# Performance work log

Hardware: AMD Instinct MI355X
Metric: run time of the kernel (lower is better)

Reference implementation:

```python
import jax, jax.numpy as jnp
import numpy as np

EMBED_DIM = 1024
NUM_HEADS = 16
HEAD_DIM = EMBED_DIM // NUM_HEADS
ALPHA = 0.5  # mirror_bias['alpha'] default


def setup_inputs() -> dict:
    key = jax.random.key(0)
    k_x, k_m, kq, kk, kv, ko = jax.random.split(key, 6)
    B, S = 2, 2048
    x = jax.random.normal(k_x, (B, S, EMBED_DIM), dtype=jnp.float32)
    mask = jax.random.bernoulli(k_m, 0.1, (B, S))  # True = masked-out key (padding)
    # xavier_uniform for square [E,E]: limit = sqrt(6/(E+E))
    lim = float(np.sqrt(6.0 / (EMBED_DIM + EMBED_DIM)))
    Wq = jax.random.uniform(kq, (EMBED_DIM, EMBED_DIM), jnp.float32, -lim, lim)
    Wk = jax.random.uniform(kk, (EMBED_DIM, EMBED_DIM), jnp.float32, -lim, lim)
    Wv = jax.random.uniform(kv, (EMBED_DIM, EMBED_DIM), jnp.float32, -lim, lim)
    Wo = jax.random.uniform(ko, (EMBED_DIM, EMBED_DIM), jnp.float32, -lim, lim)
    return {"x": x, "Wq": Wq, "Wk": Wk, "Wv": Wv, "Wo": Wo, "mask": mask}


def _heads(t, B, S):
    # [B,S,E] -> [B,H,S,D]
    return t.reshape(B, S, NUM_HEADS, HEAD_DIM).transpose(0, 2, 1, 3)


def reference(x, Wq, Wk, Wv, Wo, mask):
    B, S, E = x.shape
    # nn.Linear(bias=False): y = x @ W.T
    q = _heads(x @ Wq.T, B, S)
    k = _heads(x @ Wk.T, B, S)
    v = _heads(x @ Wv.T, B, S)
    scores = jnp.einsum('bhqd,bhkd->bhqk', q, k) / jnp.sqrt(jnp.float32(HEAD_DIM))
    # mirror positional bias: target j = S-1-i
    i_idx = jnp.arange(S)[:, None]
    j_idx = jnp.arange(S)[None, :]
    dist = jnp.abs(j_idx - (S - 1 - i_idx)).astype(jnp.float32)
    bias = -ALPHA * (dist / jnp.float32(S))  # [S_q, S_k]
    scores = scores + bias[None, None, :, :]
    # bool 2D mask -> key padding mask [B,1,1,S_k], True = -inf
    scores = jnp.where(mask[:, None, None, :], -jnp.inf, scores)
    attn = jax.nn.softmax(scores, axis=-1)
    out = jnp.einsum('bhqk,bhkd->bhqd', attn, v)
    out = out.transpose(0, 2, 1, 3).reshape(B, S, E)
    return out @ Wo.T
```

## Files before the change

### kernel.cpp

```cpp
#include <hip/hip_runtime.h>

typedef unsigned short u16;
typedef unsigned int u32;
typedef unsigned long long u64;
typedef __attribute__((ext_vector_type(8))) short bf16x8;
typedef __attribute__((ext_vector_type(4))) float f32x4;
typedef __attribute__((ext_vector_type(2))) unsigned int u32x2;
typedef __attribute__((ext_vector_type(4))) unsigned int u32x4;

#define MFMA16(A, B, C) __builtin_amdgcn_mfma_f32_16x16x32_bf16(A, B, C, 0, 0, 0)

__device__ __forceinline__ u16 f2bf(float f) {
  union { float f; unsigned u; } x; x.f = f;
  unsigned r = x.u + 0x7fffu + ((x.u >> 16) & 1u);
  return (u16)(r >> 16);
}

__device__ __forceinline__ u32 pack_bf2(float a, float b) {
  u32 r;
  asm("v_cvt_pk_bf16_f32 %0, %1, %2" : "=v"(r) : "v"(a), "v"(b));
  return r;
}

__device__ __forceinline__ void gload_lds16(const u16* g, u16* l) {
  __builtin_amdgcn_global_load_lds((const __attribute__((address_space(1))) void*)g,
                                   (__attribute__((address_space(3))) void*)l,
                                   16, 0, 0);
}

__global__ __launch_bounds__(256) void cvt_all(const float* __restrict__ x,
                                               const float* __restrict__ Wq,
                                               const float* __restrict__ Wk,
                                               const float* __restrict__ Wv,
                                               const float* __restrict__ Wo,
                                               const int* __restrict__ mask,
                                               u16* __restrict__ xb,
                                               u16* __restrict__ Wqkvb,
                                               u16* __restrict__ Wob,
                                               float* __restrict__ Mbg,
                                               int NE, int NW, int NB) {
  if ((int)blockIdx.x == NB) {
    const int t = threadIdx.x;
    const int j0 = t * 16;
    const float K3C = -8.0f * 1.44269504f;
    const float KMS = K3C - 1.0e6f;
#pragma unroll
    for (int jj = 0; jj < 16; jj += 4) {
      const int4 m4 = *(const int4*)(mask + j0 + jj);
      float4 o;
      o.x = m4.x ? KMS : K3C;
      o.y = m4.y ? KMS : K3C;
      o.z = m4.z ? KMS : K3C;
      o.w = m4.w ? KMS : K3C;
      *(float4*)(Mbg + j0 + jj) = o;
    }
    return;
  }
  const int e = (blockIdx.x * 256 + threadIdx.x) * 8;
  const float* s;
  u16* d;
  if (e < NE) { s = x + e; d = xb + e; }
  else {
    int f = e - NE;
    if (f < 3 * NW) {
      d = Wqkvb + f;
      s = (f < NW) ? Wq + f : (f < 2 * NW) ? Wk + (f - NW) : Wv + (f - 2 * NW);
    } else { f -= 3 * NW; s = Wo + f; d = Wob + f; }
  }
  const float4 a = *(const float4*)s;
  const float4 b = *(const float4*)(s + 4);
  bf16x8 o;
  o[0] = (short)f2bf(a.x); o[1] = (short)f2bf(a.y);
  o[2] = (short)f2bf(a.z); o[3] = (short)f2bf(a.w);
  o[4] = (short)f2bf(b.x); o[5] = (short)f2bf(b.y);
  o[6] = (short)f2bf(b.z); o[7] = (short)f2bf(b.w);
  *(bf16x8*)d = o;
}

__global__ __launch_bounds__(256) void gemm_qkv(const u16* __restrict__ A,
                                                const u16* __restrict__ B,
                                                u16* __restrict__ Qo,
                                                u16* __restrict__ Ko,
                                                u16* __restrict__ Vto,
                                                int M, int N, int K) {
  __shared__ alignas(16) u16 As[128 * 64];
  __shared__ alignas(16) u16 Bs[128 * 64];
  const int t = threadIdx.x;
  const int lane = t & 63, wave = t >> 6;
  const int quad = lane >> 4, l16 = lane & 15;
  const int bid = blockIdx.x;
  const int swz = (bid & 7) * 96 + (bid >> 3);
  const int m0 = (swz / 24) * 128, n0 = (swz % 24) * 128;
  const int wm = (wave >> 1) * 64, wn = (wave & 1) * 64;
  const int sx = l16 & 7;

  f32x4 acc[4][4] = {};

  for (int kk = 0; kk < K; kk += 64) {
#pragma unroll
    for (int i = 0; i < 4; i++) {
      const int c = t + i * 256;
      const int row = c >> 3, sub = c & 7;
      const int col = ((sub ^ (row & 7)) * 8);
      gload_lds16(A + (size_t)(m0 + row) * K + kk + col, As + (size_t)c * 8);
      gload_lds16(B + (size_t)(n0 + row) * K + kk + col, Bs + (size_t)c * 8);
    }
    __syncthreads();

#pragma unroll
    for (int ks = 0; ks < 2; ks++) {
      bf16x8 af[4], bfr[4];
#pragma unroll
      for (int i = 0; i < 4; i++)
        af[i] = *(const bf16x8*)(As + (wm + i * 16 + l16) * 64 +
                                 ((ks * 4 + quad) ^ sx) * 8);
#pragma unroll
      for (int j = 0; j < 4; j++)
        bfr[j] = *(const bf16x8*)(Bs + (wn + j * 16 + l16) * 64 +
                                  ((ks * 4 + quad) ^ sx) * 8);
#pragma unroll
      for (int i = 0; i < 4; i++)
#pragma unroll
        for (int j = 0; j < 4; j++)
          acc[i][j] = MFMA16(af[i], bfr[j], acc[i][j]);
    }
    __syncthreads();
  }

  const int G = ((m0 + wm) & 2047) >> 6;
#pragma unroll
  for (int j = 0; j < 4; j++) {
    const int col = n0 + wn + j * 16 + l16;
    if (col < 1024) {
#pragma unroll
      for (int i = 0; i < 4; i++)
#pragma unroll
        for (int r = 0; r < 4; r++)
          Qo[(size_t)(m0 + wm + i * 16 + quad * 4 + r) * 1024 + col] =
              f2bf(acc[i][j][r]);
    } else if (col < 2048) {
#pragma unroll
      for (int i = 0; i < 4; i++)
#pragma unroll
        for (int r = 0; r < 4; r++)
          Ko[(size_t)(m0 + wm + i * 16 + quad * 4 + r) * 1024 + (col - 1024)] =
              f2bf(acc[i][j][r]);
    } else {
      u16* base = Vto + ((size_t)(m0 >> 11) * 1024 + (col - 2048)) * 2048 + G * 64;
      const int C = 8 * (quad & 1) + 16 * (quad >> 1);
      u32x4 w0, w1;
      w0.x = pack_bf2(acc[0][j][0], acc[0][j][1]);
      w0.y = pack_bf2(acc[0][j][2], acc[0][j][3]);
      w0.z = pack_bf2(acc[1][j][0], acc[1][j][1]);
      w0.w = pack_bf2(acc[1][j][2], acc[1][j][3]);
      w1.x = pack_bf2(acc[2][j][0], acc[2][j][1]);
      w1.y = pack_bf2(acc[2][j][2], acc[2][j][3]);
      w1.z = pack_bf2(acc[3][j][0], acc[3][j][1]);
      w1.w = pack_bf2(acc[3][j][2], acc[3][j][3]);
      *(u32x4*)(base + C) = w0;
      *(u32x4*)(base + C + 32) = w1;
    }
  }
}

__global__ __launch_bounds__(256) void gemm_out(const u16* __restrict__ A,
                                                const u16* __restrict__ B,
                                                float* __restrict__ C,
                                                int M, int N, int K) {
  __shared__ alignas(16) u16 As[128 * 64];
  __shared__ alignas(16) u16 Bs[64 * 64];
  const int t = threadIdx.x;
  const int lane = t & 63, wave = t >> 6;
  const int quad = lane >> 4, l16 = lane & 15;
  const int bid = blockIdx.x;
  const int swz = (bid & 7) * 64 + (bid >> 3);
  const int m0 = (swz >> 4) * 128, n0 = (swz & 15) * 64;
  const int wm = (wave >> 1) * 64, wn = (wave & 1) * 32;
  const int sx = l16 & 7;

  f32x4 acc[4][2] = {};

  for (int kk = 0; kk < K; kk += 64) {
#pragma unroll
    for (int i = 0; i < 4; i++) {
      const int c = t + i * 256;
      const int row = c >> 3, sub = c & 7;
      gload_lds16(A + (size_t)(m0 + row) * K + kk + ((sub ^ (row & 7)) * 8),
                  As + (size_t)c * 8);
    }
#pragma unroll
    for (int i = 0; i < 2; i++) {
      const int c = t + i * 256;
      const int row = c >> 3, sub = c & 7;
      gload_lds16(B + (size_t)(n0 + row) * K + kk + ((sub ^ (row & 7)) * 8),
                  Bs + (size_t)c * 8);
    }
    __syncthreads();

#pragma unroll
    for (int ks = 0; ks < 2; ks++) {
      bf16x8 af[4], bfr[2];
#pragma unroll
      for (int i = 0; i < 4; i++)
        af[i] = *(const bf16x8*)(As + (wm + i * 16 + l16) * 64 +
                                 ((ks * 4 + quad) ^ sx) * 8);
#pragma unroll
      for (int j = 0; j < 2; j++)
        bfr[j] = *(const bf16x8*)(Bs + (wn + j * 16 + l16) * 64 +
                                  ((ks * 4 + quad) ^ sx) * 8);
#pragma unroll
      for (int i = 0; i < 4; i++)
#pragma unroll
        for (int j = 0; j < 2; j++)
          acc[i][j] = MFMA16(af[i], bfr[j], acc[i][j]);
    }
    __syncthreads();
  }

#pragma unroll
  for (int i = 0; i < 4; i++)
#pragma unroll
    for (int j = 0; j < 2; j++)
#pragma unroll
      for (int r = 0; r < 4; r++)
        C[(size_t)(m0 + wm + i * 16 + quad * 4 + r) * N + n0 + wn + j * 16 + l16] =
            acc[i][j][r];
}

__global__ __launch_bounds__(256) void attn_fwd(const u16* __restrict__ Q,
                                                const u16* __restrict__ Kb_,
                                                const u16* __restrict__ Vt,
                                                const float* __restrict__ Mb,
                                                float* __restrict__ OP0,
                                                float* __restrict__ OP1,
                                                float* __restrict__ Lp) {
  constexpr int S = 2048, E = 1024;
  __shared__ alignas(16) u16 Ks[2][64 * 64];
  __shared__ alignas(16) u16 Vs[2][64 * 64];
  __shared__ alignas(16) float Ms[1024];
  const int t = threadIdx.x;
  const int lane = t & 63, wave = t >> 6;
  const int quad = lane >> 4, l16 = lane & 15;
  const int bid = blockIdx.x;
  const int swz = (bid & 7) * 128 + (bid >> 3);
  const int xq = swz & 15, bh = (swz >> 4) & 31, sp = swz >> 9;
  const int b = bh >> 4, h = bh & 15;
  const int kbase0 = sp * 1024;
  const int q0 = xq * 128 + wave * 32;

  const int c0 = t, c1 = t + 256;
  const int kr0 = c0 >> 3, kr1 = c1 >> 3;
  const int kcol0 = ((c0 & 7) ^ (kr0 & 7)) * 8;
  const int kcol1 = ((c1 & 7) ^ (kr1 & 7)) * 8;
  const u16* kP0 = Kb_ + (size_t)(b * S + kbase0 + kr0) * E + h * 64 + kcol0;
  const u16* kP1 = Kb_ + (size_t)(b * S + kbase0 + kr1) * E + h * 64 + kcol1;
  const u16* vbase = Vt + (size_t)(b * 16 + h) * 64 * S + kbase0;
  const u16* vP0 = vbase + (size_t)kr0 * S + kcol0;
  const u16* vP1 = vbase + (size_t)kr1 * S + kcol1;

  bf16x8 aq[2][2];
#pragma unroll
  for (int qt = 0; qt < 2; qt++) {
    const u16* qp = Q + ((size_t)(b * S) + q0 + qt * 16 + l16) * E + h * 64;
    aq[qt][0] = *(const bf16x8*)(qp + quad * 8);
    aq[qt][1] = *(const bf16x8*)(qp + 32 + quad * 8);
  }

  const int sx = l16 & 7;

  float lr[2] = {};
  f32x4 accO[2][4] = {};
  const float fb0 = (float)(kbase0 + quad * 4 + q0 + l16 - 2047);

  const float K1 = 0.125f * 1.44269504f;
  const float K2 = 2.44140625e-4f * 1.44269504f;

  gload_lds16(kP0, Ks[0] + c0 * 8);
  gload_lds16(kP1, Ks[0] + c1 * 8);
  gload_lds16(vP0, Vs[0] + c0 * 8);
  gload_lds16(vP1, Vs[0] + c1 * 8);
  gload_lds16((const u16*)(Mb + b * 2048 + kbase0) + t * 8,
              (u16*)Ms + t * 8);
  __syncthreads();

  int buf = 0;
  for (int kc = 0; kc < 1024; kc += 64) {
    if (kc + 64 < 1024) {
      const int kn = kc + 64;
      gload_lds16(kP0 + (size_t)kn * E, Ks[buf ^ 1] + c0 * 8);
      gload_lds16(kP1 + (size_t)kn * E, Ks[buf ^ 1] + c1 * 8);
      gload_lds16(vP0 + kn, Vs[buf ^ 1] + c0 * 8);
      gload_lds16(vP1 + kn, Vs[buf ^ 1] + c1 * 8);
    }
    const u16* ks = Ks[buf];
    const u16* vs = Vs[buf];

    f32x4 mv[4];
#pragma unroll
    for (int T = 0; T < 4; T++)
      mv[T] = *(const f32x4*)(Ms + kc + 16 * T + quad * 4);

    bf16x8 bk[4][2];
#pragma unroll
    for (int T = 0; T < 4; T++)
#pragma unroll
      for (int dh = 0; dh < 2; dh++)
        bk[T][dh] = *(const bf16x8*)(ks + (T * 16 + l16) * 64 +
                                     ((dh * 4 + quad) ^ sx) * 8);

    f32x4 s[2][4] = {};
#pragma unroll
    for (int qt = 0; qt < 2; qt++)
#pragma unroll
      for (int T = 0; T < 4; T++) {
        s[qt][T] = MFMA16(bk[T][0], aq[qt][0], s[qt][T]);
        s[qt][T] = MFMA16(bk[T][1], aq[qt][1], s[qt][T]);
      }

    const float fbL = fb0 + (float)kc;

    u32 pw[2][2][4];
#pragma unroll
    for (int qt = 0; qt < 2; qt++)
#pragma unroll
      for (int T = 0; T < 4; T++) {
        float p[4];
#pragma unroll
        for (int r = 0; r < 4; r++) {
          const float fe = fbL + (float)(16 * T + 16 * qt + r);
          const float tv = fmaf(s[qt][T][r], K1, mv[T][r]);
          p[r] = __builtin_amdgcn_exp2f(fmaf(fabsf(fe), -K2, tv));
        }
        lr[qt] += (p[0] + p[1]) + (p[2] + p[3]);
        pw[qt][T >> 1][(T & 1) * 2 + 0] = pack_bf2(p[0], p[1]);
        pw[qt][T >> 1][(T & 1) * 2 + 1] = pack_bf2(p[2], p[3]);
      }

#pragma unroll
    for (int kst = 0; kst < 2; kst++) {
      bf16x8 bv[4];
#pragma unroll
      for (int tt = 0; tt < 4; tt++)
        bv[tt] = *(const bf16x8*)(vs + (tt * 16 + l16) * 64 +
                                  ((kst * 4 + quad) ^ sx) * 8);
#pragma unroll
      for (int qt = 0; qt < 2; qt++) {
        union { u32 w[4]; bf16x8 v; } ap;
        ap.w[0] = pw[qt][kst][0]; ap.w[1] = pw[qt][kst][1];
        ap.w[2] = pw[qt][kst][2]; ap.w[3] = pw[qt][kst][3];
#pragma unroll
        for (int tt = 0; tt < 4; tt++)
          accO[qt][tt] = MFMA16(ap.v, bv[tt], accO[qt][tt]);
      }
    }

    __syncthreads();
    buf ^= 1;
  }

  float* OP = sp ? OP1 : OP0;
#pragma unroll
  for (int qt = 0; qt < 2; qt++) {
    float l = lr[qt];
    l += __shfl_xor(l, 16);
    l += __shfl_xor(l, 32);
    if (lane < 16)
      Lp[((size_t)sp << 16) + ((size_t)bh << 11) + q0 + qt * 16 + l16] = l;
  }
#pragma unroll
  for (int qt = 0; qt < 2; qt++)
#pragma unroll
    for (int r = 0; r < 4; r++) {
      const int qg = q0 + qt * 16 + quad * 4 + r;
      const size_t row = ((size_t)bh << 11) + qg;
      float* orow = OP + row * 64;
#pragma unroll
      for (int tt = 0; tt < 4; tt++) orow[tt * 16 + l16] = accO[qt][tt][r];
    }
}

__global__ __launch_bounds__(256) void attn_merge(const float* __restrict__ OP0,
                                                  const float* __restrict__ OP1,
                                                  const float* __restrict__ Lp,
                                                  u16* __restrict__ Ao) {
  const int i = blockIdx.x * 256 + threadIdx.x;
  const int row = i >> 4;
  const int d4 = (i & 15) * 4;
  const float inv = 1.0f / (Lp[row] + Lp[65536 + row]);
  const float4 a = *(const float4*)(OP0 + (size_t)row * 64 + d4);
  const float4 c = *(const float4*)(OP1 + (size_t)row * 64 + d4);
  const int bb = row >> 15, h = (row >> 11) & 15, q = row & 2047;
  u32x2 v;
  v.x = pack_bf2((a.x + c.x) * inv, (a.y + c.y) * inv);
  v.y = pack_bf2((a.z + c.z) * inv, (a.w + c.w) * inv);
  *(u32x2*)(Ao + (size_t)((bb << 11) + q) * 1024 + h * 64 + d4) = v;
}

extern "C" void kernel_launch(void* const* d_in, const int* in_sizes, int n_in,
                              void* d_out, int out_size, void* d_ws, size_t ws_size,
                              hipStream_t stream) {
  const float* x  = (const float*)d_in[0];
  const float* Wq = (const float*)d_in[1];
  const float* Wk = (const float*)d_in[2];
  const float* Wv = (const float*)d_in[3];
  const float* Wo = (const float*)d_in[4];
  const int* mask = (const int*)d_in[5];

  const int M = 4096, N = 1024, K = 1024;
  const int NE = M * N, NW = N * K;
  const int NB = (NE + 4 * NW) / 2048;

  u16* xb    = (u16*)d_ws;
  u16* Wqkvb = xb + NE;
  u16* Wob   = Wqkvb + (size_t)3 * NW;
  u16* Qb    = Wob + NW;
  u16* Kb    = Qb + NE;
  u16* Vt    = Kb + NE;
  u16* Ao    = Vt + NE;
  float* Mbg = (float*)(Ao + NE);
  float* OP1 = Mbg + 4096;
  float* Lp  = OP1 + (size_t)65536 * 64;
  float* OP0 = (float*)d_out;

  cvt_all<<<NB + 1, 256, 0, stream>>>(x, Wq, Wk, Wv, Wo, mask,
                                      xb, Wqkvb, Wob, Mbg, NE, NW, NB);

  gemm_qkv<<<768, 256, 0, stream>>>(xb, Wqkvb, Qb, Kb, Vt, M, 3072, K);
  attn_fwd<<<1024, 256, 0, stream>>>(Qb, Kb, Vt, Mbg, OP0, OP1, Lp);
  attn_merge<<<4096, 256, 0, stream>>>(OP0, OP1, Lp, Ao);
  gemm_out<<<512, 256, 0, stream>>>(Ao, Wob, (float*)d_out, M, N, K);
}
```

Before: 194.4 us.

## Drop split-K attention and fuse normalization into attention epilogue

Each attention block now loops over all 2048 keys instead of splitting the key range in two, so the fp32 partial outputs, partial row sums and the separate merge kernel go away. Normalization and bf16 conversion happen directly in the attention epilogue. The trade-off is half as many blocks (512) on a large GPU, each with a twice-longer serial loop, in exchange for cutting the fp32 partial traffic and one launch.

```diff
diff --git a/kernel.cpp b/kernel.cpp
--- a/kernel.cpp
+++ b/kernel.cpp
@@ -231,30 +231,27 @@
                                                 const u16* __restrict__ Kb_,
                                                 const u16* __restrict__ Vt,
                                                 const float* __restrict__ Mb,
-                                                float* __restrict__ OP0,
-                                                float* __restrict__ OP1,
-                                                float* __restrict__ Lp) {
+                                                u16* __restrict__ Ao) {
   constexpr int S = 2048, E = 1024;
   __shared__ alignas(16) u16 Ks[2][64 * 64];
   __shared__ alignas(16) u16 Vs[2][64 * 64];
-  __shared__ alignas(16) float Ms[1024];
+  __shared__ alignas(16) float Ms[2048];
   const int t = threadIdx.x;
   const int lane = t & 63, wave = t >> 6;
   const int quad = lane >> 4, l16 = lane & 15;
   const int bid = blockIdx.x;
-  const int swz = (bid & 7) * 128 + (bid >> 3);
-  const int xq = swz & 15, bh = (swz >> 4) & 31, sp = swz >> 9;
+  const int swz = (bid & 7) * 64 + (bid >> 3);
+  const int xq = swz & 15, bh = swz >> 4;
   const int b = bh >> 4, h = bh & 15;
-  const int kbase0 = sp * 1024;
   const int q0 = xq * 128 + wave * 32;
 
   const int c0 = t, c1 = t + 256;
   const int kr0 = c0 >> 3, kr1 = c1 >> 3;
   const int kcol0 = ((c0 & 7) ^ (kr0 & 7)) * 8;
   const int kcol1 = ((c1 & 7) ^ (kr1 & 7)) * 8;
-  const u16* kP0 = Kb_ + (size_t)(b * S + kbase0 + kr0) * E + h * 64 + kcol0;
-  const u16* kP1 = Kb_ + (size_t)(b * S + kbase0 + kr1) * E + h * 64 + kcol1;
-  const u16* vbase = Vt + (size_t)(b * 16 + h) * 64 * S + kbase0;
+  const u16* kP0 = Kb_ + (size_t)(b * S + kr0) * E + h * 64 + kcol0;
+  const u16* kP1 = Kb_ + (size_t)(b * S + kr1) * E + h * 64 + kcol1;
+  const u16* vbase = Vt + (size_t)(b * 16 + h) * 64 * S;
   const u16* vP0 = vbase + (size_t)kr0 * S + kcol0;
   const u16* vP1 = vbase + (size_t)kr1 * S + kcol1;
 
@@ -270,7 +267,7 @@
 
   float lr[2] = {};
   f32x4 accO[2][4] = {};
-  const float fb0 = (float)(kbase0 + quad * 4 + q0 + l16 - 2047);
+  const float fb0 = (float)(quad * 4 + q0 + l16 - 2047);
 
   const float K1 = 0.125f * 1.44269504f;
   const float K2 = 2.44140625e-4f * 1.44269504f;
@@ -279,13 +276,14 @@
   gload_lds16(kP1, Ks[0] + c1 * 8);
   gload_lds16(vP0, Vs[0] + c0 * 8);
   gload_lds16(vP1, Vs[0] + c1 * 8);
-  gload_lds16((const u16*)(Mb + b * 2048 + kbase0) + t * 8,
-              (u16*)Ms + t * 8);
+  gload_lds16((const u16*)(Mb + b * 2048) + t * 8, (u16*)Ms + t * 8);
+  gload_lds16((const u16*)(Mb + b * 2048) + 2048 + t * 8,
+              (u16*)Ms + 2048 + t * 8);
   __syncthreads();
 
   int buf = 0;
-  for (int kc = 0; kc < 1024; kc += 64) {
-    if (kc + 64 < 1024) {
+  for (int kc = 0; kc < 2048; kc += 64) {
+    if (kc + 64 < 2048) {
       const int kn = kc + 64;
       gload_lds16(kP0 + (size_t)kn * E, Ks[buf ^ 1] + c0 * 8);
       gload_lds16(kP1 + (size_t)kn * E, Ks[buf ^ 1] + c1 * 8);
@@ -358,42 +356,23 @@
     buf ^= 1;
   }
 
-  float* OP = sp ? OP1 : OP0;
+  u16* aob = Ao + ((size_t)(b * 2048 + q0)) * 1024 + h * 64;
 #pragma unroll
   for (int qt = 0; qt < 2; qt++) {
     float l = lr[qt];
     l += __shfl_xor(l, 16);
     l += __shfl_xor(l, 32);
-    if (lane < 16)
-      Lp[((size_t)sp << 16) + ((size_t)bh << 11) + q0 + qt * 16 + l16] = l;
-  }
-#pragma unroll
-  for (int qt = 0; qt < 2; qt++)
+    float linv[4];
+#pragma unroll
+    for (int r = 0; r < 4; r++) linv[r] = 1.0f / __shfl(l, quad * 4 + r);
 #pragma unroll
     for (int r = 0; r < 4; r++) {
-      const int qg = q0 + qt * 16 + quad * 4 + r;
-      const size_t row = ((size_t)bh << 11) + qg;
-      float* orow = OP + row * 64;
-#pragma unroll
-      for (int tt = 0; tt < 4; tt++) orow[tt * 16 + l16] = accO[qt][tt][r];
-    }
-}
-
-__global__ __launch_bounds__(256) void attn_merge(const float* __restrict__ OP0,
-                                                  const float* __restrict__ OP1,
-                                                  const float* __restrict__ Lp,
-                                                  u16* __restrict__ Ao) {
-  const int i = blockIdx.x * 256 + threadIdx.x;
-  const int row = i >> 4;
-  const int d4 = (i & 15) * 4;
-  const float inv = 1.0f / (Lp[row] + Lp[65536 + row]);
-  const float4 a = *(const float4*)(OP0 + (size_t)row * 64 + d4);
-  const float4 c = *(const float4*)(OP1 + (size_t)row * 64 + d4);
-  const int bb = row >> 15, h = (row >> 11) & 15, q = row & 2047;
-  u32x2 v;
-  v.x = pack_bf2((a.x + c.x) * inv, (a.y + c.y) * inv);
-  v.y = pack_bf2((a.z + c.z) * inv, (a.w + c.w) * inv);
-  *(u32x2*)(Ao + (size_t)((bb << 11) + q) * 1024 + h * 64 + d4) = v;
+      u16* arow = aob + (size_t)(qt * 16 + quad * 4 + r) * 1024;
+#pragma unroll
+      for (int tt = 0; tt < 4; tt++)
+        arow[tt * 16 + l16] = f2bf(accO[qt][tt][r] * linv[r]);
+    }
+  }
 }
 
 extern "C" void kernel_launch(void* const* d_in, const int* in_sizes, int n_in,
@@ -418,15 +397,11 @@
   u16* Vt    = Kb + NE;
   u16* Ao    = Vt + NE;
   float* Mbg = (float*)(Ao + NE);
-  float* OP1 = Mbg + 4096;
-  float* Lp  = OP1 + (size_t)65536 * 64;
-  float* OP0 = (float*)d_out;
 
   cvt_all<<<NB + 1, 256, 0, stream>>>(x, Wq, Wk, Wv, Wo, mask,
                                       xb, Wqkvb, Wob, Mbg, NE, NW, NB);
 
   gemm_qkv<<<768, 256, 0, stream>>>(xb, Wqkvb, Qb, Kb, Vt, M, 3072, K);
-  attn_fwd<<<1024, 256, 0, stream>>>(Qb, Kb, Vt, Mbg, OP0, OP1, Lp);
-  attn_merge<<<4096, 256, 0, stream>>>(OP0, OP1, Lp, Ao);
+  attn_fwd<<<512, 256, 0, stream>>>(Qb, Kb, Vt, Mbg, Ao);
   gemm_out<<<512, 256, 0, stream>>>(Ao, Wob, (float*)d_out, M, N, K);
 }
```

Measured after the change: 188.5 us. 3.1% less time.
